# Performance work log

Hardware: AMD Instinct MI355X
Metric: run time of the kernel (lower is better)

Reference implementation:

```python
import jax, jax.numpy as jnp
import numpy as np

H, W, D = 1024, 1024, 128


def setup_inputs() -> dict:
    key = jax.random.key(0)
    ks = jax.random.split(key, 7)
    x = jax.random.normal(ks[0], (2, H, W), dtype=jnp.float32)
    s1 = 1.0 / np.sqrt(4.0)
    s2 = 1.0 / np.sqrt(float(D))
    W1 = jax.random.uniform(ks[1], (4, D), jnp.float32, -s1, s1)
    b1 = jax.random.uniform(ks[2], (D,), jnp.float32, -s1, s1)
    W2 = jax.random.uniform(ks[3], (D, D), jnp.float32, -s2, s2)
    b2 = jax.random.uniform(ks[4], (D,), jnp.float32, -s2, s2)
    W3 = jax.random.uniform(ks[5], (D, D), jnp.float32, -s2, s2)
    b3 = jax.random.uniform(ks[6], (D,), jnp.float32, -s2, s2)
    return dict(x=x, W1=W1, b1=b1, W2=W2, b2=b2, W3=W3, b3=b3)


def _masked_norm(v, mask):
    # normalize(v) = (v - min) / (max - min), min/max over nonzero pixels only
    big = jnp.float32(1e30)
    vmin = jnp.min(jnp.where(mask, v, big))
    vmax = jnp.max(jnp.where(mask, v, -big))
    return (v - vmin) / (vmax - vmin)


def reference(x, W1, b1, W2, b2, W3, b3):
    x0, x1 = x[0], x[1]                      # real, imag maps [H, W]
    mask = x0 != 0                            # nonzero-context pixels
    w = mask.astype(x.dtype).reshape(-1)      # [H*W] 0/1 weights

    rows = jnp.broadcast_to(jnp.arange(H, dtype=x.dtype)[:, None], (H, W))
    cols = jnp.broadcast_to(jnp.arange(W, dtype=x.dtype)[None, :], (H, W))
    nr = _masked_norm(rows, mask)
    nc = _masked_norm(cols, mask)

    # per-point features [H*W, 4]: (norm row, norm col, real, imag)
    feats = jnp.stack([nr, nc, x0, x1], axis=-1).reshape(-1, 4)

    # fc3(relu(fc2(fc1(.)))) — note: no activation between fc1 and fc2
    h = feats @ W1 + b1                       # [N, 128]
    h = h @ W2 + b2
    h = jax.nn.relu(h)
    out = h @ W3 + b3                         # [N, 128]

    # mean over nonzero points only
    return (w[:, None] * out).sum(0) / w.sum()
```

## Files before the change

kernel.cpp:

```cpp
#include <hip/hip_runtime.h>
#include <climits>

#define HH 1024
#define WW 1024
#define DD 128
#define NPIX (HH * WW)
#define NSB 256
#define NBB 512

#define RMINP 1024
#define RMAXP 1280
#define CMINP 1536
#define CMAXP 1792
#define CNTP  2048
#define PART  8192

__device__ __forceinline__ void d_stats(const float* __restrict__ x0, int blk,
                                        int tid, int* __restrict__ wsi,
                                        int (*sred)[8]) {
    const float4* x4 = (const float4*)(x0) + (size_t)blk * 1024;
    int any0, any1, any2, any3;
    int cmn = INT_MAX, cmx = -1, cnt = 0;
    int c4 = 4 * tid;
    {
        float4 v;
        bool z0, z1, z2, z3;
        #define STAT_K(K, ANY)                                                 \
            v = x4[K * 256 + tid];                                             \
            z0 = v.x != 0.f; z1 = v.y != 0.f; z2 = v.z != 0.f; z3 = v.w != 0.f;\
            ANY = (int)(z0 | z1 | z2 | z3);                                    \
            if (ANY) {                                                         \
                cmn = min(cmn, z0 ? c4 : (z1 ? c4+1 : (z2 ? c4+2 : c4+3)));    \
                cmx = max(cmx, z3 ? c4+3 : (z2 ? c4+2 : (z1 ? c4+1 : c4)));    \
            }                                                                  \
            cnt += (int)z0 + (int)z1 + (int)z2 + (int)z3;
        STAT_K(0, any0) STAT_K(1, any1) STAT_K(2, any2) STAT_K(3, any3)
        #undef STAT_K
    }
    for (int off = 32; off >= 1; off >>= 1) {
        cmn = min(cmn, __shfl_xor(cmn, off, 64));
        cmx = max(cmx, __shfl_xor(cmx, off, 64));
        cnt += __shfl_xor(cnt, off, 64);
        any0 |= __shfl_xor(any0, off, 64);
        any1 |= __shfl_xor(any1, off, 64);
        any2 |= __shfl_xor(any2, off, 64);
        any3 |= __shfl_xor(any3, off, 64);
    }
    int wave = tid >> 6;
    if ((tid & 63) == 0) {
        sred[wave][0] = cmn; sred[wave][1] = cmx; sred[wave][2] = cnt;
        sred[wave][3] = any0; sred[wave][4] = any1;
        sred[wave][5] = any2; sred[wave][6] = any3;
    }
    __syncthreads();
    if (tid == 0) {
        int a = sred[0][0], b = sred[0][1], c = sred[0][2];
        int f0 = sred[0][3], f1 = sred[0][4], f2 = sred[0][5], f3 = sred[0][6];
        for (int w = 1; w < 4; ++w) {
            a = min(a, sred[w][0]); b = max(b, sred[w][1]); c += sred[w][2];
            f0 |= sred[w][3]; f1 |= sred[w][4]; f2 |= sred[w][5]; f3 |= sred[w][6];
        }
        int r0 = blk * 4;
        wsi[RMINP + blk] = f0 ? r0 : (f1 ? r0+1 : (f2 ? r0+2 : (f3 ? r0+3 : INT_MAX)));
        wsi[RMAXP + blk] = f3 ? r0+3 : (f2 ? r0+2 : (f1 ? r0+1 : (f0 ? r0 : -1)));
        wsi[CMINP + blk] = a;
        wsi[CMAXP + blk] = b;
        wsi[CNTP  + blk] = c;
    }
}

__global__ __launch_bounds__(256) void kA(const float* __restrict__ x0,
                                          const float* __restrict__ W1,
                                          const float* __restrict__ b1,
                                          const float* __restrict__ W2,
                                          const float* __restrict__ b2,
                                          const float* __restrict__ b3,
                                          float* __restrict__ out,
                                          float* __restrict__ wsf,
                                          int* __restrict__ wsi) {
    __shared__ int sred[4][8];
    int blk = blockIdx.x, tid = threadIdx.x;
    if (blk < NSB) { d_stats(x0, blk, tid, wsi, sred); return; }
    if (tid < 128) {
        int j = tid;
        float p0 = 0.f, p1 = 0.f, p2 = 0.f, p3 = 0.f, cc = 0.f;
        #pragma unroll 8
        for (int d = 0; d < DD; ++d) {
            float w2 = W2[d * DD + j];
            p0 = fmaf(W1[0 * DD + d], w2, p0);
            p1 = fmaf(W1[1 * DD + d], w2, p1);
            p2 = fmaf(W1[2 * DD + d], w2, p2);
            p3 = fmaf(W1[3 * DD + d], w2, p3);
            cc = fmaf(b1[d],          w2, cc);
        }
        wsf[64 + 0 * DD + j] = p0;
        wsf[64 + 1 * DD + j] = p1;
        wsf[64 + 2 * DD + j] = p2;
        wsf[64 + 3 * DD + j] = p3;
        wsf[576 + j] = cc + b2[j];
        out[j] = b3[j];
    }
}

__global__ __launch_bounds__(256) void kB(const float* __restrict__ x0,
                                          const float* __restrict__ x1,
                                          float* __restrict__ wsf,
                                          const int* __restrict__ wsi) {
    __shared__ float2 sv[2048];
    __shared__ float red[256];
    __shared__ int   sred[4][4];
    __shared__ unsigned short lidx[2048];
    __shared__ int   lcnt;

    int tid = threadIdx.x, blk = blockIdx.x;
    int wv = tid >> 6;

    if (tid == 0) lcnt = 0;

    int rmn = wsi[RMINP + tid], rmx = wsi[RMAXP + tid];
    int cmn = wsi[CMINP + tid], cmx = wsi[CMAXP + tid];
    for (int off = 32; off >= 1; off >>= 1) {
        rmn = min(rmn, __shfl_xor(rmn, off, 64));
        rmx = max(rmx, __shfl_xor(rmx, off, 64));
        cmn = min(cmn, __shfl_xor(cmn, off, 64));
        cmx = max(cmx, __shfl_xor(cmx, off, 64));
    }
    if ((tid & 63) == 0) {
        sred[wv][0] = rmn; sred[wv][1] = rmx;
        sred[wv][2] = cmn; sred[wv][3] = cmx;
    }
    __syncthreads();
    rmn = min(min(sred[0][0], sred[1][0]), min(sred[2][0], sred[3][0]));
    rmx = max(max(sred[0][1], sred[1][1]), max(sred[2][1], sred[3][1]));
    cmn = min(min(sred[0][2], sred[1][2]), min(sred[2][2], sred[3][2]));
    cmx = max(max(sred[0][3], sred[1][3]), max(sred[2][3], sred[3][3]));

    const float4* x04 = (const float4*)(x0) + (size_t)blk * 512;
    const float4* x14 = (const float4*)(x1) + (size_t)blk * 512;
    float4* sv4 = (float4*)sv;
    #pragma unroll
    for (int k = 0; k < 2; ++k) {
        int i = k * 256 + tid;
        float4 va = x04[i];
        float4 vb = x14[i];
        sv4[2 * i]     = make_float4(va.x, vb.x, va.y, vb.y);
        sv4[2 * i + 1] = make_float4(va.z, vb.z, va.w, vb.w);
        int p4 = 4 * i;
        if (va.x == 0.f) { int p = atomicAdd(&lcnt, 1); lidx[p] = (unsigned short)(p4 + 0); }
        if (va.y == 0.f) { int p = atomicAdd(&lcnt, 1); lidx[p] = (unsigned short)(p4 + 1); }
        if (va.z == 0.f) { int p = atomicAdd(&lcnt, 1); lidx[p] = (unsigned short)(p4 + 2); }
        if (va.w == 0.f) { int p = atomicAdd(&lcnt, 1); lidx[p] = (unsigned short)(p4 + 3); }
    }
    __syncthreads();

    int j = tid & 127;
    int g = tid >> 7;
    int row = blk * 2 + g;
    float rs = 1.0f / (float)(rmx - rmn);
    float cs = 1.0f / (float)(cmx - cmn);
    float M2 = wsf[64 + 2 * DD + j];
    float M3 = wsf[64 + 3 * DD + j];
    float a0 = wsf[64 + 0 * DD + j] * rs;
    float a1 = wsf[64 + 1 * DD + j] * cs;
    float cp = wsf[576 + j] - (float)rmn * a0 - (float)cmn * a1;
    float a1x2 = a1 + a1;

    float rowbase = fmaf((float)row, a0, cp);
    float t = rowbase;
    float acc0 = 0.f, acc1 = 0.f;
    const float4* p = sv4 + g * 512;
    #pragma unroll 8
    for (int q = 0; q < 512; ++q) {
        float4 v = p[q];
        float d0 = fmaf(v.x, M2, fmaf(v.y, M3, t));
        float d1 = fmaf(v.z, M2, fmaf(v.w, M3, t + a1));
        acc0 += fmaxf(d0, 0.f);
        acc1 += fmaxf(d1, 0.f);
        t += a1x2;
    }
    float acc = acc0 + acc1;

    int nz = lcnt;
    for (int ii = 0; ii < nz; ++ii) {
        int px = lidx[ii];
        if ((px >> 10) == g) {
            float2 v = sv[px];
            float tp = fmaf((float)(px & 1023), a1, rowbase);
            acc -= fmaxf(fmaf(v.x, M2, fmaf(v.y, M3, tp)), 0.f);
        }
    }

    red[tid] = acc;
    __syncthreads();
    if (tid < 128) {
        wsf[PART + tid * NBB + blk] = red[tid] + red[tid + 128];
    }
}

__global__ __launch_bounds__(256) void kC(const float* __restrict__ wsf,
                                          const int* __restrict__ wsi,
                                          const float* __restrict__ W3,
                                          const float* __restrict__ b3,
                                          float* __restrict__ out) {
    __shared__ float sred[4];
    __shared__ int   cred[4];
    __shared__ float mf_sh;
    int f = blockIdx.x, tid = threadIdx.x;
    int wv = tid >> 6, lane = tid & 63;

    int c = wsi[CNTP + tid];
    for (int off = 32; off >= 1; off >>= 1) c += __shfl_xor(c, off, 64);
    if (lane == 0) cred[wv] = c;

    const float* p = wsf + PART + (size_t)f * NBB;
    float S = p[tid] + p[tid + 256];
    for (int off = 32; off >= 1; off >>= 1) S += __shfl_xor(S, off, 64);
    if (lane == 0) sred[wv] = S;
    __syncthreads();
    if (tid == 0) {
        float tot = (sred[0] + sred[1]) + (sred[2] + sred[3]);
        float cnt = (float)(cred[0] + cred[1] + cred[2] + cred[3]);
        mf_sh = tot / cnt;
    }
    __syncthreads();

    if (tid < 128) {
        float mf = mf_sh;
        atomicAdd(&out[tid], mf * W3[f * DD + tid]);
    }
}

extern "C" void kernel_launch(void* const* d_in, const int* in_sizes, int n_in,
                              void* d_out, int out_size, void* d_ws, size_t ws_size,
                              hipStream_t stream) {
    const float* x  = (const float*)d_in[0];
    const float* x0 = x;
    const float* x1 = x + NPIX;
    const float* W1 = (const float*)d_in[1];
    const float* b1 = (const float*)d_in[2];
    const float* W2 = (const float*)d_in[3];
    const float* b2 = (const float*)d_in[4];
    const float* W3 = (const float*)d_in[5];
    const float* b3 = (const float*)d_in[6];
    float* outp = (float*)d_out;
    float* wsf  = (float*)d_ws;
    int*   wsi  = (int*)d_ws;

    hipLaunchKernelGGL(kA, dim3(NSB + 1), dim3(256), 0, stream,
                       x0, W1, b1, W2, b2, b3, outp, wsf, wsi);
    hipLaunchKernelGGL(kB, dim3(NBB), dim3(256), 0, stream, x0, x1, wsf, wsi);
    hipLaunchKernelGGL(kC, dim3(DD), dim3(256), 0, stream, wsf, wsi, W3, b3, outp);
}
```

Before: 33.43 us.

## Fuse final reduction into kB via last-block ticket and retile feature loop

Removes the separate kC launch: each kB block writes its partials, bumps an atomic ticket, and the last block reduces all partials, divides by the count and does the W3 matvec directly, so the output atomics go away. The inner loop is also retiled so each thread handles 4 features over a quarter row, which reuses each LDS float4 load four times. This costs threadfences plus a serial tail in one block, and raises register pressure.

New measurement: 82.34 us. 146% more time.

```diff
diff --git a/kernel.cpp b/kernel.cpp
--- a/kernel.cpp
+++ b/kernel.cpp
@@ -13,6 +13,7 @@
 #define CMINP 1536
 #define CMAXP 1792
 #define CNTP  2048
+#define DONE  2304
 #define PART  8192
 
 __device__ __forceinline__ void d_stats(const float* __restrict__ x0, int blk,
@@ -74,13 +75,12 @@
                                           const float* __restrict__ b1,
                                           const float* __restrict__ W2,
                                           const float* __restrict__ b2,
-                                          const float* __restrict__ b3,
-                                          float* __restrict__ out,
                                           float* __restrict__ wsf,
                                           int* __restrict__ wsi) {
     __shared__ int sred[4][8];
     int blk = blockIdx.x, tid = threadIdx.x;
     if (blk < NSB) { d_stats(x0, blk, tid, wsi, sred); return; }
+    if (tid == 0) wsi[DONE] = 0;
     if (tid < 128) {
         int j = tid;
         float p0 = 0.f, p1 = 0.f, p2 = 0.f, p3 = 0.f, cc = 0.f;
@@ -98,22 +98,28 @@
         wsf[64 + 2 * DD + j] = p2;
         wsf[64 + 3 * DD + j] = p3;
         wsf[576 + j] = cc + b2[j];
-        out[j] = b3[j];
     }
 }
 
 __global__ __launch_bounds__(256) void kB(const float* __restrict__ x0,
                                           const float* __restrict__ x1,
+                                          const float* __restrict__ W3,
+                                          const float* __restrict__ b3,
+                                          float* __restrict__ out,
                                           float* __restrict__ wsf,
-                                          const int* __restrict__ wsi) {
+                                          int* __restrict__ wsi) {
     __shared__ float2 sv[2048];
-    __shared__ float red[256];
-    __shared__ int   sred[4][4];
     __shared__ unsigned short lidx[2048];
     __shared__ int   lcnt;
+    __shared__ int   sred[4][4];
+    __shared__ float fred[128][9];
+    __shared__ int   tk_sh;
+    __shared__ float s2[256];
+    __shared__ float sm[128];
+    __shared__ int   cred[4];
 
     int tid = threadIdx.x, blk = blockIdx.x;
-    int wv = tid >> 6;
+    int wv = tid >> 6, lane = tid & 63;
 
     if (tid == 0) lcnt = 0;
 
@@ -125,7 +131,7 @@
         cmn = min(cmn, __shfl_xor(cmn, off, 64));
         cmx = max(cmx, __shfl_xor(cmx, off, 64));
     }
-    if ((tid & 63) == 0) {
+    if (lane == 0) {
         sred[wv][0] = rmn; sred[wv][1] = rmx;
         sred[wv][2] = cmn; sred[wv][3] = cmx;
     }
@@ -153,81 +159,104 @@
     }
     __syncthreads();
 
-    int j = tid & 127;
-    int g = tid >> 7;
-    int row = blk * 2 + g;
+    int ft = tid & 31;
+    int rg = (tid >> 5) & 1;
+    int cq = tid >> 6;
+    int row = blk * 2 + rg;
     float rs = 1.0f / (float)(rmx - rmn);
     float cs = 1.0f / (float)(cmx - cmn);
-    float M2 = wsf[64 + 2 * DD + j];
-    float M3 = wsf[64 + 3 * DD + j];
-    float a0 = wsf[64 + 0 * DD + j] * rs;
-    float a1 = wsf[64 + 1 * DD + j] * cs;
-    float cp = wsf[576 + j] - (float)rmn * a0 - (float)cmn * a1;
-    float a1x2 = a1 + a1;
-
-    float rowbase = fmaf((float)row, a0, cp);
-    float t = rowbase;
-    float acc0 = 0.f, acc1 = 0.f;
-    const float4* p = sv4 + g * 512;
-    #pragma unroll 8
-    for (int q = 0; q < 512; ++q) {
+
+    float M2[4], M3[4], a1v[4], a1x2[4], rb[4], tA[4], tB[4], acc0[4], acc1[4];
+    #pragma unroll
+    for (int k = 0; k < 4; ++k) {
+        int f = ft + 32 * k;
+        M2[k] = wsf[64 + 2 * DD + f];
+        M3[k] = wsf[64 + 3 * DD + f];
+        float a0 = wsf[64 + 0 * DD + f] * rs;
+        float a1 = wsf[64 + 1 * DD + f] * cs;
+        float cp = wsf[576 + f] - (float)rmn * a0 - (float)cmn * a1;
+        rb[k]  = fmaf((float)row, a0, cp);
+        a1v[k] = a1;
+        tA[k]  = fmaf((float)(cq * 256), a1, rb[k]);
+        tB[k]  = tA[k] + a1;
+        a1x2[k] = a1 + a1;
+        acc0[k] = 0.f; acc1[k] = 0.f;
+    }
+
+    const float4* p = sv4 + rg * 512 + cq * 128;
+    #pragma unroll 4
+    for (int q = 0; q < 128; ++q) {
         float4 v = p[q];
-        float d0 = fmaf(v.x, M2, fmaf(v.y, M3, t));
-        float d1 = fmaf(v.z, M2, fmaf(v.w, M3, t + a1));
-        acc0 += fmaxf(d0, 0.f);
-        acc1 += fmaxf(d1, 0.f);
-        t += a1x2;
-    }
-    float acc = acc0 + acc1;
+        #pragma unroll
+        for (int k = 0; k < 4; ++k) {
+            float d0 = fmaf(v.x, M2[k], fmaf(v.y, M3[k], tA[k]));
+            float d1 = fmaf(v.z, M2[k], fmaf(v.w, M3[k], tB[k]));
+            acc0[k] += fmaxf(d0, 0.f);
+            acc1[k] += fmaxf(d1, 0.f);
+            tA[k] += a1x2[k];
+            tB[k] += a1x2[k];
+        }
+    }
 
     int nz = lcnt;
     for (int ii = 0; ii < nz; ++ii) {
         int px = lidx[ii];
-        if ((px >> 10) == g) {
+        int zr = px >> 10, zc = px & 1023;
+        if (zr == rg && (zc >> 8) == cq) {
             float2 v = sv[px];
-            float tp = fmaf((float)(px & 1023), a1, rowbase);
-            acc -= fmaxf(fmaf(v.x, M2, fmaf(v.y, M3, tp)), 0.f);
-        }
-    }
-
-    red[tid] = acc;
+            #pragma unroll
+            for (int k = 0; k < 4; ++k) {
+                float tp = fmaf((float)zc, a1v[k], rb[k]);
+                acc0[k] -= fmaxf(fmaf(v.x, M2[k], fmaf(v.y, M3[k], tp)), 0.f);
+            }
+        }
+    }
+
+    #pragma unroll
+    for (int k = 0; k < 4; ++k)
+        fred[ft + 32 * k][rg * 4 + cq] = acc0[k] + acc1[k];
     __syncthreads();
     if (tid < 128) {
-        wsf[PART + tid * NBB + blk] = red[tid] + red[tid + 128];
-    }
-}
-
-__global__ __launch_bounds__(256) void kC(const float* __restrict__ wsf,
-                                          const int* __restrict__ wsi,
-                                          const float* __restrict__ W3,
-                                          const float* __restrict__ b3,
-                                          float* __restrict__ out) {
-    __shared__ float sred[4];
-    __shared__ int   cred[4];
-    __shared__ float mf_sh;
-    int f = blockIdx.x, tid = threadIdx.x;
-    int wv = tid >> 6, lane = tid & 63;
-
+        const float* fr = fred[tid];
+        float s = ((fr[0] + fr[1]) + (fr[2] + fr[3]))
+                + ((fr[4] + fr[5]) + (fr[6] + fr[7]));
+        wsf[PART + (size_t)tid * NBB + blk] = s;
+    }
+    __threadfence();
+    __syncthreads();
+    if (tid == 0) tk_sh = atomicAdd(&wsi[DONE], 1);
+    __syncthreads();
+    if (tk_sh != NBB - 1) return;
+
+    __threadfence();
     int c = wsi[CNTP + tid];
     for (int off = 32; off >= 1; off >>= 1) c += __shfl_xor(c, off, 64);
     if (lane == 0) cred[wv] = c;
 
-    const float* p = wsf + PART + (size_t)f * NBB;
-    float S = p[tid] + p[tid + 256];
-    for (int off = 32; off >= 1; off >>= 1) S += __shfl_xor(S, off, 64);
-    if (lane == 0) sred[wv] = S;
-    __syncthreads();
-    if (tid == 0) {
-        float tot = (sred[0] + sred[1]) + (sred[2] + sred[3]);
-        float cnt = (float)(cred[0] + cred[1] + cred[2] + cred[3]);
-        mf_sh = tot / cnt;
-    }
-    __syncthreads();
-
-    if (tid < 128) {
-        float mf = mf_sh;
-        atomicAdd(&out[tid], mf * W3[f * DD + tid]);
-    }
+    {
+        const float4* pf = (const float4*)(wsf + PART + (size_t)(tid >> 1) * NBB
+                                           + (tid & 1) * 256);
+        float sx = 0.f, sy = 0.f, sz = 0.f, sw = 0.f;
+        #pragma unroll 8
+        for (int q = 0; q < 64; ++q) {
+            float4 v = pf[q];
+            sx += v.x; sy += v.y; sz += v.z; sw += v.w;
+        }
+        s2[tid] = (sx + sy) + (sz + sw);
+    }
+    __syncthreads();
+    float cntf = (float)(cred[0] + cred[1] + cred[2] + cred[3]);
+    if (tid < 128) sm[tid] = (s2[2 * tid] + s2[2 * tid + 1]) / cntf;
+    __syncthreads();
+
+    int col = tid & 127, h = tid >> 7;
+    float o = 0.f;
+    #pragma unroll 8
+    for (int d = h * 64; d < h * 64 + 64; ++d)
+        o = fmaf(sm[d], W3[d * DD + col], o);
+    s2[tid] = o;
+    __syncthreads();
+    if (tid < 128) out[tid] = b3[tid] + s2[tid] + s2[tid + 128];
 }
 
 extern "C" void kernel_launch(void* const* d_in, const int* in_sizes, int n_in,
@@ -247,7 +276,7 @@
     int*   wsi  = (int*)d_ws;
 
     hipLaunchKernelGGL(kA, dim3(NSB + 1), dim3(256), 0, stream,
-                       x0, W1, b1, W2, b2, b3, outp, wsf, wsi);
-    hipLaunchKernelGGL(kB, dim3(NBB), dim3(256), 0, stream, x0, x1, wsf, wsi);
-    hipLaunchKernelGGL(kC, dim3(DD), dim3(256), 0, stream, wsf, wsi, W3, b3, outp);
-}
+                       x0, W1, b1, W2, b2, wsf, wsi);
+    hipLaunchKernelGGL(kB, dim3(NBB), dim3(256), 0, stream,
+                       x0, x1, W3, b3, outp, wsf, wsi);
+}
```
